# Performance work log

Hardware: AMD Instinct MI355X
Metric: run time of the kernel (lower is better)

The kernel has to match this reference:

```python
import jax, jax.numpy as jnp
import numpy as np

DIM, KEY_DIM, HEADS, RATIO, RES = 384, 32, 8, 4, 14
NH_KD = KEY_DIM * HEADS            # 256
D = RATIO * KEY_DIM                # 128
DH = D * HEADS                     # 1024
H_QKV = DH + 2 * NH_KD             # 1536
N_OFF = RES * RES                  # 196 unique (|dy|,|dx|) offsets
EPS = 1e-5


def _bn(x, g, b, m, v):
    # inference-mode BatchNorm2d over channel dim 1 of [B,C,H,W]
    s = (g * jax.lax.rsqrt(v + EPS))[None, :, None, None]
    return x * s + (b - m * g * jax.lax.rsqrt(v + EPS))[None, :, None, None]


def setup_inputs() -> dict:
    key = jax.random.key(0)
    ks = jax.random.split(key, 8)
    B = 256
    x = jax.random.normal(ks[0], (B, DIM, RES, RES), dtype=jnp.float32)
    # 1x1 qkv conv weight [out,in]
    qkv_w = jax.random.normal(ks[1], (H_QKV, DIM), dtype=jnp.float32) * 0.02
    # depthwise 3x3 conv on q channels [C,1,3,3]
    dw_w = jax.random.normal(ks[2], (NH_KD, 1, 3, 3), dtype=jnp.float32) * 0.1
    # 1x1 proj conv weight [out,in]
    proj_w = jax.random.normal(ks[3], (DIM, DH), dtype=jnp.float32) * 0.02
    attention_biases = jax.random.normal(ks[4], (HEADS, N_OFF), dtype=jnp.float32) * 0.1

    def bn_params(k, c):
        k1, k2 = jax.random.split(k)
        return (1.0 + 0.1 * jax.random.normal(k1, (c,), dtype=jnp.float32),
                0.1 * jax.random.normal(k2, (c,), dtype=jnp.float32),
                jnp.zeros((c,), jnp.float32), jnp.ones((c,), jnp.float32))
    qkv_g, qkv_b, qkv_m, qkv_v = bn_params(ks[5], H_QKV)
    dw_g, dw_b, dw_m, dw_v = bn_params(ks[6], NH_KD)
    proj_g, proj_b, proj_m, proj_v = bn_params(ks[7], DIM)

    # relative position bias index map [N, N], via (|dy|, |dx|) -> |dy|*RES + |dx|
    pts = np.arange(RES)
    yy, xx = np.meshgrid(pts, pts, indexing='ij')
    coords = np.stack([yy.ravel(), xx.ravel()], axis=1)  # [N,2]
    dy = np.abs(coords[:, None, 0] - coords[None, :, 0])
    dx = np.abs(coords[:, None, 1] - coords[None, :, 1])
    bias_idxs = jnp.asarray(dy * RES + dx, dtype=jnp.int32)  # [N,N]

    return dict(x=x, qkv_w=qkv_w, qkv_g=qkv_g, qkv_b=qkv_b, qkv_m=qkv_m, qkv_v=qkv_v,
                dw_w=dw_w, dw_g=dw_g, dw_b=dw_b, dw_m=dw_m, dw_v=dw_v,
                proj_w=proj_w, proj_g=proj_g, proj_b=proj_b, proj_m=proj_m, proj_v=proj_v,
                attention_biases=attention_biases, bias_idxs=bias_idxs)


def reference(x, qkv_w, qkv_g, qkv_b, qkv_m, qkv_v,
              dw_w, dw_g, dw_b, dw_m, dw_v,
              proj_w, proj_g, proj_b, proj_m, proj_v,
              attention_biases, bias_idxs):
    B, _, Hs, Ws = x.shape
    N = Hs * Ws
    scale = KEY_DIM ** -0.5
    # qkv: 1x1 conv + BN
    qkv = _bn(jnp.einsum('bchw,oc->bohw', x, qkv_w), qkv_g, qkv_b, qkv_m, qkv_v)
    q, k, v = jnp.split(qkv, [NH_KD, 2 * NH_KD], axis=1)
    # depthwise 3x3 conv + BN on q
    q = jax.lax.conv_general_dilated(q, dw_w, (1, 1), 'SAME',
                                     feature_group_count=NH_KD,
                                     dimension_numbers=('NCHW', 'OIHW', 'NCHW'))
    q = _bn(q, dw_g, dw_b, dw_m, dw_v)
    q = q.reshape(B, HEADS, KEY_DIM, N)
    k = k.reshape(B, HEADS, KEY_DIM, N)
    v = v.reshape(B, HEADS, D, N)
    ab = attention_biases[:, bias_idxs]                     # [heads, N, N]
    attn = jnp.einsum('bhdn,bhdm->bhnm', q, k) * scale + ab[None]
    attn = jax.nn.softmax(attn, axis=-1)
    out = jnp.einsum('bhdm,bhnm->bhdn', v, attn).reshape(B, DH, Hs, Ws)
    # proj: ReLU -> 1x1 conv -> BN
    out = jnp.einsum('bchw,oc->bohw', jax.nn.relu(out), proj_w)
    out = _bn(out, proj_g, proj_b, proj_m, proj_v)
    return out
```

## Files before the change

kernel.cpp:

```cpp
#include <hip/hip_runtime.h>
#include <hip/hip_bf16.h>
#include <stdint.h>

#define DIM 384
#define KEY_DIM 32
#define HEADS 8
#define RES 14
#define NTOK 196
#define NH_KD 256
#define DD 128
#define DHF 1024
#define H_QKV 1536
#define BATCH 256
#define QSTR 224
#define EPS_BN 1e-5f
#define LOG2E 1.4426950408889634f
#define QSCALE 0.25501860152f
#define PSTR 232

typedef unsigned short ushort_t;
typedef __attribute__((ext_vector_type(8))) short short8;
typedef __attribute__((ext_vector_type(4))) float floatx4;

__device__ __forceinline__ ushort_t f2bf(float f) {
  union { float f; unsigned int u; } v; v.f = f;
  unsigned int u = v.u;
  unsigned int r = (u + 0x7FFFu + ((u >> 16) & 1u)) >> 16;
  return (ushort_t)r;
}
__device__ __forceinline__ float bf2f(ushort_t h) {
  union { unsigned int u; float f; } v; v.u = ((unsigned int)h) << 16;
  return v.f;
}
__device__ __forceinline__ void async_copy16(const ushort_t* g, ushort_t* l) {
  __builtin_amdgcn_global_load_lds((const __attribute__((address_space(1))) void*)g,
                                   (__attribute__((address_space(3))) void*)l, 16, 0, 0);
}

__global__ void k_prep_x(const float* __restrict__ x, ushort_t* __restrict__ xb) {
  __shared__ float tile[64][65];
  const int b = blockIdx.y;
  const int c0 = blockIdx.x * 64;
  const int t = threadIdx.x;
  const int tr = t >> 6;
  const int tc = t & 63;
  for (int n0 = 0; n0 < QSTR; n0 += 64) {
    __syncthreads();
    #pragma unroll
    for (int k = 0; k < 16; ++k) {
      int r = k * 4 + tr;
      int n = n0 + tc;
      tile[r][tc] = (n < NTOK) ? x[((size_t)b * DIM + c0 + r) * NTOK + n] : 0.f;
    }
    __syncthreads();
    #pragma unroll
    for (int k = 0; k < 16; ++k) {
      int nl = k * 4 + tr;
      int n = n0 + nl;
      if (n < QSTR) xb[((size_t)b * QSTR + n) * DIM + c0 + tc] = f2bf(tile[tc][nl]);
    }
  }
}

__global__ void k_prep_w(const float* __restrict__ qkv_w, const float* __restrict__ proj_w,
                         ushort_t* __restrict__ wqkvb, ushort_t* __restrict__ wprojb) {
  int i = blockIdx.x * 256 + threadIdx.x;
  const int nA = H_QKV * DIM;
  const int nB = DIM * DHF;
  if (i < nA) wqkvb[i] = f2bf(qkv_w[i]);
  else if (i < nA + nB) wprojb[i - nA] = f2bf(proj_w[i - nA]);
}

__global__ void k_prep_abC(const float* __restrict__ biases, const int* __restrict__ idxs,
                           float* __restrict__ abgC) {
  int tid = blockIdx.x * 256 + threadIdx.x;
  if (tid >= HEADS * 13 * 13 * 64) return;
  const int l = tid & 63;
  int rem = tid >> 6;
  const int j = rem % 13; rem /= 13;
  const int rt = rem % 13;
  const int h = rem / 13;
  const int quad = l >> 4, l15 = l & 15;
  const int m = j * 16 + l15;
  #pragma unroll
  for (int r = 0; r < 4; ++r) {
    int n = rt * 16 + quad * 4 + r; if (n > NTOK - 1) n = NTOK - 1;
    float v = (m < NTOK) ? biases[h * NTOK + idxs[n * NTOK + m]] * LOG2E : -1e30f;
    abgC[(size_t)tid * 4 + r] = v;
  }
}

template<int KDIM, bool OUTF32>
__global__ __launch_bounds__(256, 2) void k_gemm(
    const ushort_t* __restrict__ A, const ushort_t* __restrict__ B,
    const float* __restrict__ bn_g, const float* __restrict__ bn_b,
    const float* __restrict__ bn_m, const float* __restrict__ bn_v,
    void* __restrict__ out) {
  __shared__ ushort_t sA[128 * 32];
  __shared__ ushort_t sB[128 * 32];
  const int n0 = blockIdx.x * 128;
  const int o0 = blockIdx.y * 128;
  const int t = threadIdx.x;
  const int w = t >> 6;
  const int l = t & 63;
  const int lr = l >> 2;
  const int ls = l & 3;
  const int arow0 = w * 32 + lr;
  const size_t aoff0 = (size_t)(o0 + arow0) * KDIM + ls * 8;
  const size_t aoff1 = aoff0 + (size_t)16 * KDIM;
  const size_t boff0 = (size_t)(n0 + arow0) * KDIM + ls * 8;
  const size_t boff1 = boff0 + (size_t)16 * KDIM;
  ushort_t* sA_w = sA + w * 1024;
  ushort_t* sB_w = sB + w * 1024;

  floatx4 acc[4][4];
  const floatx4 zero4 = {0.f, 0.f, 0.f, 0.f};
  #pragma unroll
  for (int i = 0; i < 4; ++i)
    #pragma unroll
    for (int j = 0; j < 4; ++j) acc[i][j] = zero4;

  const int wr = (w >> 1) * 64;
  const int wc = (w & 1) * 64;
  const int quad = l >> 4;
  const int l15 = l & 15;

  for (int kk = 0; kk < KDIM; kk += 32) {
    __syncthreads();
    async_copy16(A + aoff0 + kk, sA_w);
    async_copy16(A + aoff1 + kk, sA_w + 512);
    async_copy16(B + boff0 + kk, sB_w);
    async_copy16(B + boff1 + kk, sB_w + 512);
    __syncthreads();
    short8 af[4], bfv[4];
    #pragma unroll
    for (int i = 0; i < 4; ++i)
      af[i] = *(const short8*)(sA + (wr + i * 16 + l15) * 32 + quad * 8);
    #pragma unroll
    for (int j = 0; j < 4; ++j)
      bfv[j] = *(const short8*)(sB + (wc + j * 16 + l15) * 32 + quad * 8);
    #pragma unroll
    for (int i = 0; i < 4; ++i)
      #pragma unroll
      for (int j = 0; j < 4; ++j)
        acc[i][j] = __builtin_amdgcn_mfma_f32_16x16x32_bf16(af[i], bfv[j], acc[i][j], 0, 0, 0);
  }

  unsigned bq[4], nn[4];
  #pragma unroll
  for (int j = 0; j < 4; ++j) {
    const unsigned gn = n0 + wc + j * 16 + l15;
    bq[j] = gn / QSTR;
    nn[j] = gn - bq[j] * QSTR;
  }
  #pragma unroll
  for (int i = 0; i < 4; ++i) {
    #pragma unroll
    for (int r = 0; r < 4; ++r) {
      const int o = o0 + wr + i * 16 + quad * 4 + r;
      const float s = bn_g[o] * rsqrtf(bn_v[o] + EPS_BN);
      const float tt = bn_b[o] - bn_m[o] * s;
      #pragma unroll
      for (int j = 0; j < 4; ++j) {
        const float val = acc[i][j][r] * s + tt;
        if (OUTF32) {
          if (nn[j] < NTOK)
            ((float*)out)[((size_t)bq[j] * DIM + o) * NTOK + nn[j]] = val;
        } else {
          ((ushort_t*)out)[((size_t)bq[j] * H_QKV + o) * QSTR + nn[j]] = f2bf(val);
        }
      }
    }
  }
}

__global__ __launch_bounds__(64) void k_dwq(
    const ushort_t* __restrict__ qkvb, const float* __restrict__ dw_w,
    const float* __restrict__ dg, const float* __restrict__ db,
    const float* __restrict__ dm, const float* __restrict__ dv,
    ushort_t* __restrict__ qt, ushort_t* __restrict__ kt) {
  __shared__ ushort_t sq[32 * QSTR];
  __shared__ ushort_t sk[32 * QSTR];
  const int bh = blockIdx.x;
  const int b = bh >> 3, h = bh & 7;
  const int l = threadIdx.x;
  const int d = l & 31;
  const int half = l >> 5;
  const int c = h * 32 + d;
  float wv[9];
  #pragma unroll
  for (int tp = 0; tp < 9; ++tp) wv[tp] = dw_w[c * 9 + tp];
  const float s = dg[c] * rsqrtf(dv[c] + EPS_BN);
  const float tt = db[c] - dm[c] * s;
  const uint4* gq = (const uint4*)(qkvb + ((size_t)b * H_QKV + h * 32) * QSTR);
  const uint4* gk = (const uint4*)(qkvb + ((size_t)b * H_QKV + NH_KD + h * 32) * QSTR);
  uint4* lq = (uint4*)sq;
  uint4* lk = (uint4*)sk;
  for (int i = l; i < 896; i += 64) { lq[i] = gq[i]; lk[i] = gk[i]; }
  __syncthreads();
  for (int i = 0; i < 98; ++i) {
    const int n = i * 2 + half;
    const int y = n / 14, x = n - y * 14;
    float a = 0.f;
    #pragma unroll
    for (int dy = -1; dy <= 1; ++dy)
      #pragma unroll
      for (int dx = -1; dx <= 1; ++dx) {
        const int yy = y + dy, xx = x + dx;
        if (yy >= 0 && yy < 14 && xx >= 0 && xx < 14)
          a += bf2f(sq[d * QSTR + yy * 14 + xx]) * wv[(dy + 1) * 3 + (dx + 1)];
      }
    const float outv = (a * s + tt) * QSCALE;
    qt[((size_t)bh * NTOK + n) * 32 + d] = f2bf(outv);
    kt[((size_t)bh * NTOK + n) * 32 + d] = sk[d * QSTR + n];
  }
}

__global__ __launch_bounds__(256, 2) void k_attn(
    const ushort_t* __restrict__ qt, const ushort_t* __restrict__ kt,
    const ushort_t* __restrict__ qkvb, const float* __restrict__ abgC,
    ushort_t* __restrict__ rbuf) {
  __shared__ ushort_t sV[64 * PSTR];
  __shared__ ushort_t sP[4 * 16 * PSTR];
  const int id = blockIdx.x;
  const int dhalf = id & 1;
  const int bh = id >> 1;
  const int b = bh >> 3, h = bh & 7;
  const int t = threadIdx.x;
  const int w = t >> 6, l = t & 63;
  const int quad = l >> 4, l15 = l & 15;

  {
    const ushort_t* vsrc = qkvb + ((size_t)b * H_QKV + 2 * NH_KD + h * DD + dhalf * 64) * QSTR;
    for (int i = t; i < 2048; i += 256) {
      const int row = i >> 5, col = i & 31;
      if (col < 28)
        *(uint4*)(sV + row * PSTR + col * 8) = *(const uint4*)(vsrc + (size_t)row * QSTR + col * 8);
    }
    if (t < 128) {
      const int wb = t >> 5, rr = (t >> 1) & 15, hf = t & 1;
      *(uint4*)(sP + wb * 16 * PSTR + rr * PSTR + 208 + hf * 8) = make_uint4(0, 0, 0, 0);
    }
  }
  short8 kf[13];
  const ushort_t* kbase = kt + (size_t)bh * NTOK * 32;
  #pragma unroll
  for (int j = 0; j < 13; ++j) {
    int krow = j * 16 + l15; if (krow > NTOK - 1) krow = NTOK - 1;
    kf[j] = *(const short8*)(kbase + krow * 32 + quad * 8);
  }
  __syncthreads();

  const ushort_t* qbase = qt + (size_t)bh * NTOK * 32;
  ushort_t* myP = sP + w * 16 * PSTR;
  const floatx4 zero4 = {0.f, 0.f, 0.f, 0.f};

  for (int rt = w; rt < 13; rt += 4) {
    int qrow = rt * 16 + l15; if (qrow > NTOK - 1) qrow = NTOK - 1;
    const short8 aq = *(const short8*)(qbase + qrow * 32 + quad * 8);
    const floatx4* cb = (const floatx4*)(abgC) + ((size_t)(h * 13 + rt) * 13) * 64 + l;
    floatx4 lg[13];
    #pragma unroll
    for (int j = 0; j < 13; ++j)
      lg[j] = __builtin_amdgcn_mfma_f32_16x16x32_bf16(aq, kf[j], cb[j * 64], 0, 0, 0);

    float mx[4] = {-3e38f, -3e38f, -3e38f, -3e38f};
    #pragma unroll
    for (int j = 0; j < 13; ++j)
      #pragma unroll
      for (int r = 0; r < 4; ++r) mx[r] = fmaxf(mx[r], lg[j][r]);
    #pragma unroll
    for (int r = 0; r < 4; ++r) {
      float m = mx[r];
      m = fmaxf(m, __shfl_xor(m, 1));
      m = fmaxf(m, __shfl_xor(m, 2));
      m = fmaxf(m, __shfl_xor(m, 4));
      m = fmaxf(m, __shfl_xor(m, 8));
      mx[r] = m;
    }
    float sum[4] = {0.f, 0.f, 0.f, 0.f};
    #pragma unroll
    for (int j = 0; j < 13; ++j)
      #pragma unroll
      for (int r = 0; r < 4; ++r) {
        const float e = exp2f(lg[j][r] - mx[r]);
        lg[j][r] = e;
        sum[r] += e;
      }
    #pragma unroll
    for (int r = 0; r < 4; ++r) {
      float sv = sum[r];
      sv += __shfl_xor(sv, 1);
      sv += __shfl_xor(sv, 2);
      sv += __shfl_xor(sv, 4);
      sv += __shfl_xor(sv, 8);
      sum[r] = 1.f / sv;
    }
    #pragma unroll
    for (int j = 0; j < 13; ++j)
      #pragma unroll
      for (int r = 0; r < 4; ++r)
        myP[(quad * 4 + r) * PSTR + j * 16 + l15] = f2bf(lg[j][r] * sum[r]);

    short8 aA[7];
    #pragma unroll
    for (int ks = 0; ks < 7; ++ks)
      aA[ks] = *(const short8*)(myP + l15 * PSTR + ks * 32 + quad * 8);
    #pragma unroll
    for (int ct = 0; ct < 4; ++ct) {
      floatx4 a = zero4;
      #pragma unroll
      for (int ks = 0; ks < 7; ++ks) {
        const short8 bv = *(const short8*)(sV + (ct * 16 + l15) * PSTR + ks * 32 + quad * 8);
        a = __builtin_amdgcn_mfma_f32_16x16x32_bf16(aA[ks], bv, a, 0, 0, 0);
      }
      #pragma unroll
      for (int r = 0; r < 4; ++r) {
        const float v = a[r];
        myP[(quad * 4 + r) * PSTR + ct * 16 + l15] = f2bf(v > 0.f ? v : 0.f);
      }
    }
    #pragma unroll
    for (int p = 0; p < 4; ++p) {
      const int nl = p * 4 + quad;
      const int n = rt * 16 + nl;
      if (n < NTOK) {
        const uint2 val = *(const uint2*)(myP + nl * PSTR + l15 * 4);
        *(uint2*)(rbuf + ((size_t)b * QSTR + n) * DHF + h * DD + dhalf * 64 + l15 * 4) = val;
      }
    }
  }
}

extern "C" void kernel_launch(void* const* d_in, const int* in_sizes, int n_in,
                              void* d_out, int out_size, void* d_ws, size_t ws_size,
                              hipStream_t stream) {
  const float* x      = (const float*)d_in[0];
  const float* qkv_w  = (const float*)d_in[1];
  const float* qkv_g  = (const float*)d_in[2];
  const float* qkv_b  = (const float*)d_in[3];
  const float* qkv_m  = (const float*)d_in[4];
  const float* qkv_v  = (const float*)d_in[5];
  const float* dw_w   = (const float*)d_in[6];
  const float* dw_g   = (const float*)d_in[7];
  const float* dw_b   = (const float*)d_in[8];
  const float* dw_m   = (const float*)d_in[9];
  const float* dw_v   = (const float*)d_in[10];
  const float* proj_w = (const float*)d_in[11];
  const float* proj_g = (const float*)d_in[12];
  const float* proj_b = (const float*)d_in[13];
  const float* proj_m = (const float*)d_in[14];
  const float* proj_v = (const float*)d_in[15];
  const float* ab     = (const float*)d_in[16];
  const int*   idxs   = (const int*)d_in[17];
  (void)in_sizes; (void)n_in; (void)out_size;

  char* p = (char*)d_ws;
  ushort_t* wqkvb  = (ushort_t*)p; p += (size_t)H_QKV * DIM * 2;
  ushort_t* wprojb = (ushort_t*)p; p += (size_t)DIM * DHF * 2;
  float*    abgC   = (float*)p;    p += (size_t)HEADS * 13 * 13 * 64 * 4 * 4;
  const size_t fixed = (size_t)(p - (char*)d_ws);
  const size_t perb = (size_t)QSTR * DIM * 2 + (size_t)H_QKV * QSTR * 2
                    + 2 * (size_t)HEADS * NTOK * 32 * 2 + (size_t)QSTR * DHF * 2;
  int cb = 8;
  const int cands[6] = {256, 128, 64, 32, 16, 8};
  for (int i = 0; i < 6; ++i) {
    if (fixed + (size_t)cands[i] * perb <= ws_size) { cb = cands[i]; break; }
  }
  ushort_t* xb   = (ushort_t*)p;
  ushort_t* qkvb = xb + (size_t)cb * QSTR * DIM;
  ushort_t* qt   = qkvb + (size_t)cb * H_QKV * QSTR;
  ushort_t* kt   = qt + (size_t)cb * HEADS * NTOK * 32;
  ushort_t* rbuf = kt + (size_t)cb * HEADS * NTOK * 32;

  k_prep_w<<<(H_QKV * DIM + DIM * DHF + 255) / 256, 256, 0, stream>>>(qkv_w, proj_w, wqkvb, wprojb);
  k_prep_abC<<<(HEADS * 13 * 13 * 64 + 255) / 256, 256, 0, stream>>>(ab, idxs, abgC);

  const int NT = cb * QSTR / 128;
  for (int b0 = 0; b0 < BATCH; b0 += cb) {
    k_prep_x<<<dim3(6, cb), 256, 0, stream>>>(x + (size_t)b0 * DIM * NTOK, xb);
    k_gemm<DIM, false><<<dim3(NT, 12), 256, 0, stream>>>(wqkvb, xb, qkv_g, qkv_b, qkv_m, qkv_v, qkvb);
    k_dwq<<<cb * HEADS, 64, 0, stream>>>(qkvb, dw_w, dw_g, dw_b, dw_m, dw_v, qt, kt);
    k_attn<<<cb * HEADS * 2, 256, 0, stream>>>(qt, kt, qkvb, abgC, rbuf);
    k_gemm<DHF, true><<<dim3(NT, 3), 256, 0, stream>>>(wprojb, rbuf, proj_g, proj_b, proj_m, proj_v,
                                                       (float*)d_out + (size_t)b0 * DIM * NTOK);
  }
}
```

Baseline: 685.8 us.

## Keep attention probabilities in registers via transposed MFMA and drop max subtraction

```diff
diff --git a/kernel.cpp b/kernel.cpp
--- a/kernel.cpp
+++ b/kernel.cpp
@@ -17,6 +17,7 @@
 #define LOG2E 1.4426950408889634f
 #define QSCALE 0.25501860152f
 #define PSTR 232
+#define OSTR 72
 
 typedef unsigned short ushort_t;
 typedef __attribute__((ext_vector_type(8))) short short8;
@@ -31,6 +32,10 @@
 __device__ __forceinline__ float bf2f(ushort_t h) {
   union { unsigned int u; float f; } v; v.u = ((unsigned int)h) << 16;
   return v.f;
+}
+__device__ __forceinline__ unsigned pk2bf(float lo, float hi) {
+  __hip_bfloat162 h2 = __float22bfloat162_rn(make_float2(lo, hi));
+  union { __hip_bfloat162 h; unsigned u; } c; c.h = h2; return c.u;
 }
 __device__ __forceinline__ void async_copy16(const ushort_t* g, ushort_t* l) {
   __builtin_amdgcn_global_load_lds((const __attribute__((address_space(1))) void*)g,
@@ -71,8 +76,8 @@
   else if (i < nA + nB) wprojb[i - nA] = f2bf(proj_w[i - nA]);
 }
 
-__global__ void k_prep_abC(const float* __restrict__ biases, const int* __restrict__ idxs,
-                           float* __restrict__ abgC) {
+__global__ void k_prep_abT(const float* __restrict__ biases, const int* __restrict__ idxs,
+                           float* __restrict__ abgT) {
   int tid = blockIdx.x * 256 + threadIdx.x;
   if (tid >= HEADS * 13 * 13 * 64) return;
   const int l = tid & 63;
@@ -81,12 +86,12 @@
   const int rt = rem % 13;
   const int h = rem / 13;
   const int quad = l >> 4, l15 = l & 15;
-  const int m = j * 16 + l15;
+  int n = rt * 16 + l15; if (n > NTOK - 1) n = NTOK - 1;
   #pragma unroll
   for (int r = 0; r < 4; ++r) {
-    int n = rt * 16 + quad * 4 + r; if (n > NTOK - 1) n = NTOK - 1;
+    const int m = j * 16 + quad * 4 + r;
     float v = (m < NTOK) ? biases[h * NTOK + idxs[n * NTOK + m]] * LOG2E : -1e30f;
-    abgC[(size_t)tid * 4 + r] = v;
+    abgT[(size_t)tid * 4 + r] = v;
   }
 }
 
@@ -174,7 +179,7 @@
   }
 }
 
-__global__ __launch_bounds__(64) void k_dwq(
+__global__ __launch_bounds__(128) void k_dwq(
     const ushort_t* __restrict__ qkvb, const float* __restrict__ dw_w,
     const float* __restrict__ dg, const float* __restrict__ db,
     const float* __restrict__ dm, const float* __restrict__ dv,
@@ -183,9 +188,9 @@
   __shared__ ushort_t sk[32 * QSTR];
   const int bh = blockIdx.x;
   const int b = bh >> 3, h = bh & 7;
-  const int l = threadIdx.x;
-  const int d = l & 31;
-  const int half = l >> 5;
+  const int t = threadIdx.x;
+  const int d = t & 31;
+  const int grp = t >> 5;
   const int c = h * 32 + d;
   float wv[9];
   #pragma unroll
@@ -196,10 +201,10 @@
   const uint4* gk = (const uint4*)(qkvb + ((size_t)b * H_QKV + NH_KD + h * 32) * QSTR);
   uint4* lq = (uint4*)sq;
   uint4* lk = (uint4*)sk;
-  for (int i = l; i < 896; i += 64) { lq[i] = gq[i]; lk[i] = gk[i]; }
+  for (int i = t; i < 896; i += 128) { lq[i] = gq[i]; lk[i] = gk[i]; }
   __syncthreads();
-  for (int i = 0; i < 98; ++i) {
-    const int n = i * 2 + half;
+  for (int i = 0; i < 49; ++i) {
+    const int n = i * 4 + grp;
     const int y = n / 14, x = n - y * 14;
     float a = 0.f;
     #pragma unroll
@@ -216,12 +221,12 @@
   }
 }
 
-__global__ __launch_bounds__(256, 2) void k_attn(
+__global__ __launch_bounds__(256, 4) void k_attn(
     const ushort_t* __restrict__ qt, const ushort_t* __restrict__ kt,
-    const ushort_t* __restrict__ qkvb, const float* __restrict__ abgC,
+    const ushort_t* __restrict__ qkvb, const float* __restrict__ abgT,
     ushort_t* __restrict__ rbuf) {
   __shared__ ushort_t sV[64 * PSTR];
-  __shared__ ushort_t sP[4 * 16 * PSTR];
+  __shared__ ushort_t sO[4 * 16 * OSTR];
   const int id = blockIdx.x;
   const int dhalf = id & 1;
   const int bh = id >> 1;
@@ -232,14 +237,9 @@
 
   {
     const ushort_t* vsrc = qkvb + ((size_t)b * H_QKV + 2 * NH_KD + h * DD + dhalf * 64) * QSTR;
-    for (int i = t; i < 2048; i += 256) {
-      const int row = i >> 5, col = i & 31;
-      if (col < 28)
-        *(uint4*)(sV + row * PSTR + col * 8) = *(const uint4*)(vsrc + (size_t)row * QSTR + col * 8);
-    }
-    if (t < 128) {
-      const int wb = t >> 5, rr = (t >> 1) & 15, hf = t & 1;
-      *(uint4*)(sP + wb * 16 * PSTR + rr * PSTR + 208 + hf * 8) = make_uint4(0, 0, 0, 0);
+    for (int i = t; i < 1792; i += 256) {
+      const int row = i / 28, col = i - row * 28;
+      *(uint4*)(sV + row * PSTR + col * 8) = *(const uint4*)(vsrc + (size_t)row * QSTR + col * 8);
     }
   }
   short8 kf[13];
@@ -252,82 +252,85 @@
   __syncthreads();
 
   const ushort_t* qbase = qt + (size_t)bh * NTOK * 32;
-  ushort_t* myP = sP + w * 16 * PSTR;
+  ushort_t* sOw = sO + w * 16 * OSTR;
   const floatx4 zero4 = {0.f, 0.f, 0.f, 0.f};
+  const int srcA = ((l & 16) << 1) + l15;
+  const int srcB = srcA + 16;
+  const int tsel = l >> 5;
 
   for (int rt = w; rt < 13; rt += 4) {
     int qrow = rt * 16 + l15; if (qrow > NTOK - 1) qrow = NTOK - 1;
     const short8 aq = *(const short8*)(qbase + qrow * 32 + quad * 8);
-    const floatx4* cb = (const floatx4*)(abgC) + ((size_t)(h * 13 + rt) * 13) * 64 + l;
+    const floatx4* cbT = (const floatx4*)(abgT) + ((size_t)(h * 13 + rt) * 13) * 64 + l;
     floatx4 lg[13];
     #pragma unroll
     for (int j = 0; j < 13; ++j)
-      lg[j] = __builtin_amdgcn_mfma_f32_16x16x32_bf16(aq, kf[j], cb[j * 64], 0, 0, 0);
-
-    float mx[4] = {-3e38f, -3e38f, -3e38f, -3e38f};
-    #pragma unroll
-    for (int j = 0; j < 13; ++j)
+      lg[j] = __builtin_amdgcn_mfma_f32_16x16x32_bf16(kf[j], aq, cbT[j * 64], 0, 0, 0);
+
+    float s0 = 0.f, s1 = 0.f, s2 = 0.f, s3 = 0.f;
+    #pragma unroll
+    for (int j = 0; j < 13; ++j) {
+      lg[j][0] = exp2f(lg[j][0]); s0 += lg[j][0];
+      lg[j][1] = exp2f(lg[j][1]); s1 += lg[j][1];
+      lg[j][2] = exp2f(lg[j][2]); s2 += lg[j][2];
+      lg[j][3] = exp2f(lg[j][3]); s3 += lg[j][3];
+    }
+    float ssum = (s0 + s1) + (s2 + s3);
+    ssum += __shfl_xor(ssum, 16, 64);
+    ssum += __shfl_xor(ssum, 32, 64);
+    const float inv = 1.f / ssum;
+
+    unsigned plo[14], phi[14];
+    #pragma unroll
+    for (int j = 0; j < 13; ++j) {
+      plo[j] = pk2bf(lg[j][0], lg[j][1]);
+      phi[j] = pk2bf(lg[j][2], lg[j][3]);
+    }
+    plo[13] = 0; phi[13] = 0;
+
+    floatx4 acc[4];
+    #pragma unroll
+    for (int ct = 0; ct < 4; ++ct) acc[ct] = zero4;
+    #pragma unroll
+    for (int ks = 0; ks < 7; ++ks) {
+      const unsigned a0 = __shfl((int)plo[2 * ks], srcA, 64);
+      const unsigned a1 = __shfl((int)phi[2 * ks], srcA, 64);
+      const unsigned a2 = __shfl((int)plo[2 * ks], srcB, 64);
+      const unsigned a3 = __shfl((int)phi[2 * ks], srcB, 64);
+      const unsigned b0 = __shfl((int)plo[2 * ks + 1], srcA, 64);
+      const unsigned b1 = __shfl((int)phi[2 * ks + 1], srcA, 64);
+      const unsigned b2 = __shfl((int)plo[2 * ks + 1], srcB, 64);
+      const unsigned b3 = __shfl((int)phi[2 * ks + 1], srcB, 64);
+      union { unsigned u[4]; short8 s; } pf;
+      pf.u[0] = tsel ? b0 : a0;
+      pf.u[1] = tsel ? b1 : a1;
+      pf.u[2] = tsel ? b2 : a2;
+      pf.u[3] = tsel ? b3 : a3;
       #pragma unroll
-      for (int r = 0; r < 4; ++r) mx[r] = fmaxf(mx[r], lg[j][r]);
-    #pragma unroll
-    for (int r = 0; r < 4; ++r) {
-      float m = mx[r];
-      m = fmaxf(m, __shfl_xor(m, 1));
-      m = fmaxf(m, __shfl_xor(m, 2));
-      m = fmaxf(m, __shfl_xor(m, 4));
-      m = fmaxf(m, __shfl_xor(m, 8));
-      mx[r] = m;
-    }
-    float sum[4] = {0.f, 0.f, 0.f, 0.f};
-    #pragma unroll
-    for (int j = 0; j < 13; ++j)
-      #pragma unroll
-      for (int r = 0; r < 4; ++r) {
-        const float e = exp2f(lg[j][r] - mx[r]);
-        lg[j][r] = e;
-        sum[r] += e;
+      for (int ct = 0; ct < 4; ++ct) {
+        const short8 bv = *(const short8*)(sV + (ct * 16 + l15) * PSTR + ks * 32 + quad * 8);
+        acc[ct] = __builtin_amdgcn_mfma_f32_16x16x32_bf16(bv, pf.s, acc[ct], 0, 0, 0);
       }
-    #pragma unroll
-    for (int r = 0; r < 4; ++r) {
-      float sv = sum[r];
-      sv += __shfl_xor(sv, 1);
-      sv += __shfl_xor(sv, 2);
-      sv += __shfl_xor(sv, 4);
-      sv += __shfl_xor(sv, 8);
-      sum[r] = 1.f / sv;
-    }
-    #pragma unroll
-    for (int j = 0; j < 13; ++j)
-      #pragma unroll
-      for (int r = 0; r < 4; ++r)
-        myP[(quad * 4 + r) * PSTR + j * 16 + l15] = f2bf(lg[j][r] * sum[r]);
-
-    short8 aA[7];
-    #pragma unroll
-    for (int ks = 0; ks < 7; ++ks)
-      aA[ks] = *(const short8*)(myP + l15 * PSTR + ks * 32 + quad * 8);
+    }
+
     #pragma unroll
     for (int ct = 0; ct < 4; ++ct) {
-      floatx4 a = zero4;
-      #pragma unroll
-      for (int ks = 0; ks < 7; ++ks) {
-        const short8 bv = *(const short8*)(sV + (ct * 16 + l15) * PSTR + ks * 32 + quad * 8);
-        a = __builtin_amdgcn_mfma_f32_16x16x32_bf16(aA[ks], bv, a, 0, 0, 0);
-      }
-      #pragma unroll
-      for (int r = 0; r < 4; ++r) {
-        const float v = a[r];
-        myP[(quad * 4 + r) * PSTR + ct * 16 + l15] = f2bf(v > 0.f ? v : 0.f);
-      }
-    }
-    #pragma unroll
-    for (int p = 0; p < 4; ++p) {
-      const int nl = p * 4 + quad;
-      const int n = rt * 16 + nl;
-      if (n < NTOK) {
-        const uint2 val = *(const uint2*)(myP + nl * PSTR + l15 * 4);
-        *(uint2*)(rbuf + ((size_t)b * QSTR + n) * DHF + h * DD + dhalf * 64 + l15 * 4) = val;
-      }
+      const float o0 = fmaxf(acc[ct][0] * inv, 0.f);
+      const float o1 = fmaxf(acc[ct][1] * inv, 0.f);
+      const float o2 = fmaxf(acc[ct][2] * inv, 0.f);
+      const float o3 = fmaxf(acc[ct][3] * inv, 0.f);
+      *(unsigned*)(sOw + l15 * OSTR + ct * 16 + quad * 4)     = pk2bf(o0, o1);
+      *(unsigned*)(sOw + l15 * OSTR + ct * 16 + quad * 4 + 2) = pk2bf(o2, o3);
+    }
+    #pragma unroll
+    for (int p = 0; p < 2; ++p) {
+      const int i = l + p * 64;
+      const int row = i >> 3;
+      const int col = i & 7;
+      const int n = rt * 16 + row;
+      const uint4 val = *(const uint4*)(sOw + row * OSTR + col * 8);
+      if (n < NTOK)
+        *(uint4*)(rbuf + ((size_t)b * QSTR + n) * DHF + h * DD + dhalf * 64 + col * 8) = val;
     }
   }
 }
@@ -358,7 +361,7 @@
   char* p = (char*)d_ws;
   ushort_t* wqkvb  = (ushort_t*)p; p += (size_t)H_QKV * DIM * 2;
   ushort_t* wprojb = (ushort_t*)p; p += (size_t)DIM * DHF * 2;
-  float*    abgC   = (float*)p;    p += (size_t)HEADS * 13 * 13 * 64 * 4 * 4;
+  float*    abgT   = (float*)p;    p += (size_t)HEADS * 13 * 13 * 64 * 4 * 4;
   const size_t fixed = (size_t)(p - (char*)d_ws);
   const size_t perb = (size_t)QSTR * DIM * 2 + (size_t)H_QKV * QSTR * 2
                     + 2 * (size_t)HEADS * NTOK * 32 * 2 + (size_t)QSTR * DHF * 2;
@@ -374,14 +377,14 @@
   ushort_t* rbuf = kt + (size_t)cb * HEADS * NTOK * 32;
 
   k_prep_w<<<(H_QKV * DIM + DIM * DHF + 255) / 256, 256, 0, stream>>>(qkv_w, proj_w, wqkvb, wprojb);
-  k_prep_abC<<<(HEADS * 13 * 13 * 64 + 255) / 256, 256, 0, stream>>>(ab, idxs, abgC);
+  k_prep_abT<<<(HEADS * 13 * 13 * 64 + 255) / 256, 256, 0, stream>>>(ab, idxs, abgT);
 
   const int NT = cb * QSTR / 128;
   for (int b0 = 0; b0 < BATCH; b0 += cb) {
     k_prep_x<<<dim3(6, cb), 256, 0, stream>>>(x + (size_t)b0 * DIM * NTOK, xb);
     k_gemm<DIM, false><<<dim3(NT, 12), 256, 0, stream>>>(wqkvb, xb, qkv_g, qkv_b, qkv_m, qkv_v, qkvb);
-    k_dwq<<<cb * HEADS, 64, 0, stream>>>(qkvb, dw_w, dw_g, dw_b, dw_m, dw_v, qt, kt);
-    k_attn<<<cb * HEADS * 2, 256, 0, stream>>>(qt, kt, qkvb, abgC, rbuf);
+    k_dwq<<<cb * HEADS, 128, 0, stream>>>(qkvb, dw_w, dw_g, dw_b, dw_m, dw_v, qt, kt);
+    k_attn<<<cb * HEADS * 2, 256, 0, stream>>>(qt, kt, qkvb, abgT, rbuf);
     k_gemm<DHF, true><<<dim3(NT, 3), 256, 0, stream>>>(wprojb, rbuf, proj_g, proj_b, proj_m, proj_v,
                                                        (float*)d_out + (size_t)b0 * DIM * NTOK);
   }
```

Result: slower. 911.2 us (+32.9%).
